# Kernel tuning notes

Measured on AMD Instinct MI355X. Metric: run time of the kernel, lower is better.

Reference implementation:

```python
import jax, jax.numpy as jnp
import numpy as np

D = 256      # input channels
DK = 64      # key/query/value channels
BS, W, H = 8, 64, 64


def setup_inputs() -> dict:
    key = jax.random.key(0)
    k1, k2, k3, k4 = jax.random.split(key, 4)
    v = jax.random.normal(k1, (BS, D, W, H), dtype=jnp.float32)
    # conv1x1 weights collapse to plain matrices over the channel dim
    Wqkv = jax.random.normal(k2, (3 * DK, D), dtype=jnp.float32) * 0.02
    Wout = jax.random.normal(k3, (D, DK), dtype=jnp.float32) * 0.02
    gamma = jax.random.normal(k4, (1,), dtype=jnp.float32)  # original inits to 0; nonzero for a non-degenerate baseline
    return {"v": v, "Wqkv": Wqkv, "Wout": Wout, "gamma": gamma}


def reference(v, Wqkv, Wout, gamma):
    bs, c, w, h = v.shape
    n = w * h
    d_k = Wout.shape[1]
    x = v.reshape(bs, c, n)                      # (b, c, n)
    qkv = jnp.einsum('oc,bcn->bon', Wqkv, x)      # 1x1 conv == channel matmul
    q = qkv[:, :d_k]                              # (b, dk, n)
    k = qkv[:, d_k:2 * d_k]
    val = qkv[:, 2 * d_k:]
    s = jnp.einsum('bdi,bdj->bij', q, k)          # (b, n, n) = query^T key
    beta = jax.nn.softmax(s, axis=2)              # exp(s - logsumexp(s, axis=2))
    y = jnp.einsum('bdi,bij->bdj', val, beta)     # bmm(value, beta)
    o = jnp.einsum('od,bdn->bon', Wout, y) * gamma[0] + x
    return o.reshape(bs, c, w, h)
```

## Files before the change

kernel.cpp:

```cpp
#include <hip/hip_runtime.h>

typedef unsigned short ushort_t;
typedef __bf16 bf16x8 __attribute__((ext_vector_type(8)));
typedef short short4v __attribute__((ext_vector_type(4)));
typedef float f32x4 __attribute__((ext_vector_type(4)));
typedef unsigned int uint4v __attribute__((ext_vector_type(4)));
typedef unsigned int uint2v __attribute__((ext_vector_type(2)));

#define NTOK 4096
#define DMODEL 256
#define DK 64
#define BS 8

__device__ __forceinline__ ushort_t f2bf(float f) {
  unsigned u = __builtin_bit_cast(unsigned, f);
  u += 0x7fffu + ((u >> 16) & 1u);
  return (ushort_t)(u >> 16);
}
__device__ __forceinline__ float bf2f(ushort_t s) {
  return __builtin_bit_cast(float, ((unsigned)s) << 16);
}
__device__ __forceinline__ bf16x8 lds_frag(const ushort_t* p) {
  return __builtin_bit_cast(bf16x8, *(const uint4v*)p);
}
__device__ __forceinline__ f32x4 mfma16(short4v a, short4v b, f32x4 c) {
#if defined(__HIP_DEVICE_COMPILE__)
#if __has_builtin(__builtin_amdgcn_mfma_f32_16x16x16bf16_1k)
  return __builtin_amdgcn_mfma_f32_16x16x16bf16_1k(a, b, c, 0, 0, 0);
#else
  typedef __bf16 bf16x4 __attribute__((ext_vector_type(4)));
  return __builtin_amdgcn_mfma_f32_16x16x16_bf16(__builtin_bit_cast(bf16x4, a),
                                                 __builtin_bit_cast(bf16x4, b), c, 0, 0, 0);
#endif
#else
  (void)a; (void)b;
  return c;
#endif
}

__global__ __launch_bounds__(256) void k_convert(const float* __restrict__ Wqkv,
                                                 const float* __restrict__ Wout,
                                                 ushort_t* __restrict__ Wb,
                                                 ushort_t* __restrict__ Woutb) {
  int i = blockIdx.x * 256 + threadIdx.x;
  if (i < 3 * DK * DMODEL) {
    Wb[i] = f2bf(Wqkv[i]);
  } else {
    int j = i - 3 * DK * DMODEL;
    Woutb[j] = f2bf(Wout[j]);
  }
}

__global__ __launch_bounds__(256) void k_transpose(const float* __restrict__ x,
                                                   ushort_t* __restrict__ xT) {
  const int b = blockIdx.z;
  const int c0 = blockIdx.y * 64;
  const int n0 = blockIdx.x * 64;
  const int tid = threadIdx.x;
  __shared__ __align__(16) ushort_t t[64 * 72];
  const float* xb = x + (size_t)b * DMODEL * NTOK;
  ushort_t* xTb = xT + (size_t)b * NTOK * DMODEL;
#pragma unroll
  for (int kr = 0; kr < 2; kr++) {
    int s = tid + 256 * kr;
    int c = s >> 3, ns = (s & 7) * 8;
    const float* src = xb + (size_t)(c0 + c) * NTOK + n0 + ns;
    f32x4 a = *(const f32x4*)src;
    f32x4 bq = *(const f32x4*)(src + 4);
    uint4v o;
    o.x = (unsigned)f2bf(a[0]) | ((unsigned)f2bf(a[1]) << 16);
    o.y = (unsigned)f2bf(a[2]) | ((unsigned)f2bf(a[3]) << 16);
    o.z = (unsigned)f2bf(bq[0]) | ((unsigned)f2bf(bq[1]) << 16);
    o.w = (unsigned)f2bf(bq[2]) | ((unsigned)f2bf(bq[3]) << 16);
    *(uint4v*)(t + c * 72 + ns) = o;
  }
  __syncthreads();
#pragma unroll
  for (int kr = 0; kr < 2; kr++) {
    int s = tid + 256 * kr;
    int n = s >> 3, cs = (s & 7) * 8;
    unsigned e0 = t[(cs + 0) * 72 + n], e1 = t[(cs + 1) * 72 + n];
    unsigned e2 = t[(cs + 2) * 72 + n], e3 = t[(cs + 3) * 72 + n];
    unsigned e4 = t[(cs + 4) * 72 + n], e5 = t[(cs + 5) * 72 + n];
    unsigned e6 = t[(cs + 6) * 72 + n], e7 = t[(cs + 7) * 72 + n];
    uint4v o;
    o.x = e0 | (e1 << 16); o.y = e2 | (e3 << 16);
    o.z = e4 | (e5 << 16); o.w = e6 | (e7 << 16);
    *(uint4v*)(xTb + (size_t)(n0 + n) * DMODEL + c0 + cs) = o;
  }
}

__global__ __launch_bounds__(256) void k_qkv(const ushort_t* __restrict__ xT,
                                             const ushort_t* __restrict__ W,
                                             ushort_t* __restrict__ QT,
                                             ushort_t* __restrict__ KT,
                                             ushort_t* __restrict__ Vv) {
  const int b = blockIdx.y;
  const int n0 = blockIdx.x * 64;
  const int tid = threadIdx.x;
  const int lane = tid & 63, wv = tid >> 6;
  const int quad = lane >> 4, l15 = lane & 15;
  __shared__ __align__(16) ushort_t lw[192 * 40];
  __shared__ __align__(16) ushort_t lx[64 * 40];
  f32x4 acc[3][4];
  const f32x4 zero4 = {0.f, 0.f, 0.f, 0.f};
#pragma unroll
  for (int i = 0; i < 3; i++)
#pragma unroll
    for (int j = 0; j < 4; j++) acc[i][j] = zero4;

  const ushort_t* xTb = xT + ((size_t)b * NTOK + n0) * DMODEL;

  for (int c0 = 0; c0 < DMODEL; c0 += 32) {
    __syncthreads();
#pragma unroll
    for (int kr = 0; kr < 3; kr++) {
      int s = tid + 256 * kr;
      int o = s >> 2, cs = (s & 3) * 8;
      *(uint4v*)(lw + o * 40 + cs) = *(const uint4v*)(W + o * DMODEL + c0 + cs);
    }
    {
      int n = tid >> 2, cs = (tid & 3) * 8;
      *(uint4v*)(lx + n * 40 + cs) = *(const uint4v*)(xTb + (size_t)n * DMODEL + c0 + cs);
    }
    __syncthreads();
    bf16x8 bb[4];
#pragma unroll
    for (int nt = 0; nt < 4; nt++) bb[nt] = lds_frag(lx + (nt * 16 + l15) * 40 + quad * 8);
#pragma unroll
    for (int mt = 0; mt < 3; mt++) {
      bf16x8 a = lds_frag(lw + (wv * 48 + mt * 16 + l15) * 40 + quad * 8);
#pragma unroll
      for (int nt = 0; nt < 4; nt++)
        acc[mt][nt] = __builtin_amdgcn_mfma_f32_16x16x32_bf16(a, bb[nt], acc[mt][nt], 0, 0, 0);
    }
  }
#pragma unroll
  for (int mt = 0; mt < 3; mt++) {
    int o = wv * 48 + mt * 16 + quad * 4;
#pragma unroll
    for (int nt = 0; nt < 4; nt++) {
      int n = n0 + nt * 16 + l15;
      f32x4 v4 = acc[mt][nt];
      if (o < 128) {
        ushort_t* dst = (o < 64) ? (QT + ((size_t)b * NTOK + n) * DK + o)
                                 : (KT + ((size_t)b * NTOK + n) * DK + (o - 64));
        uint2v ww;
        ww.x = (unsigned)f2bf(v4[0]) | ((unsigned)f2bf(v4[1]) << 16);
        ww.y = (unsigned)f2bf(v4[2]) | ((unsigned)f2bf(v4[3]) << 16);
        *(uint2v*)dst = ww;
      } else {
        int d = o - 128;
#pragma unroll
        for (int r = 0; r < 4; r++)
          Vv[((size_t)b * DK + d + r) * NTOK + n] = f2bf(v4[r]);
      }
    }
  }
}

__global__ __launch_bounds__(256) void k_stats(const ushort_t* __restrict__ QT,
                                               const ushort_t* __restrict__ KT,
                                               ushort_t* __restrict__ Vv) {
  const int b = blockIdx.y;
  const int i0 = blockIdx.x * 64;
  const int tid = threadIdx.x;
  const int lane = tid & 63, wv = tid >> 6;
  const int quad = lane >> 4, l15 = lane & 15;
  __shared__ __align__(16) ushort_t lq[64 * 72];
  __shared__ __align__(16) ushort_t lk[2][64 * 72];
  __shared__ float lrr[64];
  const ushort_t* QTb = QT + ((size_t)b * NTOK + i0) * DK;
  const ushort_t* KTb = KT + (size_t)b * NTOK * DK;
#pragma unroll
  for (int kr = 0; kr < 2; kr++) {
    int s = tid + 256 * kr;
    int row = s >> 3, ds = (s & 7) * 8;
    *(uint4v*)(lq + row * 72 + ds) = *(const uint4v*)(QTb + (size_t)row * DK + ds);
    *(uint4v*)(lk[0] + row * 72 + ds) = *(const uint4v*)(KTb + (size_t)row * DK + ds);
  }
  __syncthreads();
  bf16x8 a0 = lds_frag(lq + (wv * 16 + l15) * 72 + quad * 8);
  bf16x8 a1 = lds_frag(lq + (wv * 16 + l15) * 72 + 32 + quad * 8);
  float lsum0 = 0.f, lsum1 = 0.f, lsum2 = 0.f, lsum3 = 0.f;
  const f32x4 zero4 = {0.f, 0.f, 0.f, 0.f};
  for (int it = 0; it < 64; it++) {
    if (it + 1 < 64) {
      const ushort_t* src = KTb + (size_t)(it + 1) * 64 * DK;
      ushort_t* dstb = lk[(it + 1) & 1];
#pragma unroll
      for (int kr = 0; kr < 2; kr++) {
        int s = tid + 256 * kr;
        int row = s >> 3, ds = (s & 7) * 8;
        *(uint4v*)(dstb + row * 72 + ds) = *(const uint4v*)(src + (size_t)row * DK + ds);
      }
    }
    const ushort_t* kb = lk[it & 1];
#pragma unroll
    for (int nt = 0; nt < 4; nt++) {
      bf16x8 b0 = lds_frag(kb + (nt * 16 + l15) * 72 + quad * 8);
      bf16x8 b1 = lds_frag(kb + (nt * 16 + l15) * 72 + 32 + quad * 8);
      f32x4 s4 = __builtin_amdgcn_mfma_f32_16x16x32_bf16(a0, b0, zero4, 0, 0, 0);
      s4 = __builtin_amdgcn_mfma_f32_16x16x32_bf16(a1, b1, s4, 0, 0, 0);
      lsum0 += __expf(s4[0]);
      lsum1 += __expf(s4[1]);
      lsum2 += __expf(s4[2]);
      lsum3 += __expf(s4[3]);
    }
    __syncthreads();
  }
#pragma unroll
  for (int off = 1; off < 16; off <<= 1) {
    lsum0 += __shfl_xor(lsum0, off);
    lsum1 += __shfl_xor(lsum1, off);
    lsum2 += __shfl_xor(lsum2, off);
    lsum3 += __shfl_xor(lsum3, off);
  }
  if (l15 == 0) {
    int rr = wv * 16 + quad * 4;
    lrr[rr + 0] = 1.0f / lsum0;
    lrr[rr + 1] = 1.0f / lsum1;
    lrr[rr + 2] = 1.0f / lsum2;
    lrr[rr + 3] = 1.0f / lsum3;
  }
  __syncthreads();
  {
    int d = tid >> 2, ig = (tid & 3) * 16;
    ushort_t* vp = Vv + ((size_t)b * DK + d) * NTOK + i0 + ig;
    uint4v v0 = *(const uint4v*)vp;
    uint4v v1 = *(const uint4v*)(vp + 8);
    uint4v o0, o1;
    unsigned* vi0 = (unsigned*)&v0;
    unsigned* vi1 = (unsigned*)&v1;
    unsigned* oo0 = (unsigned*)&o0;
    unsigned* oo1 = (unsigned*)&o1;
#pragma unroll
    for (int w = 0; w < 4; w++) {
      float e0 = bf2f((ushort_t)(vi0[w] & 0xffff)) * lrr[ig + 2 * w];
      float e1 = bf2f((ushort_t)(vi0[w] >> 16)) * lrr[ig + 2 * w + 1];
      oo0[w] = (unsigned)f2bf(e0) | ((unsigned)f2bf(e1) << 16);
      float e2 = bf2f((ushort_t)(vi1[w] & 0xffff)) * lrr[ig + 8 + 2 * w];
      float e3 = bf2f((ushort_t)(vi1[w] >> 16)) * lrr[ig + 8 + 2 * w + 1];
      oo1[w] = (unsigned)f2bf(e2) | ((unsigned)f2bf(e3) << 16);
    }
    *(uint4v*)vp = o0;
    *(uint4v*)(vp + 8) = o1;
  }
}

__global__ __launch_bounds__(256) void k_attn(const ushort_t* __restrict__ QT,
                                              const ushort_t* __restrict__ KT,
                                              const ushort_t* __restrict__ Vv,
                                              const ushort_t* __restrict__ Wout,
                                              const float* __restrict__ gammap,
                                              const float* __restrict__ x,
                                              float* __restrict__ outp) {
  const int b = blockIdx.y;
  const int j0 = blockIdx.x * 64;
  const int tid = threadIdx.x;
  const int lane = tid & 63, wv = tid >> 6;
  const int quad = lane >> 4, l15 = lane & 15;

  __shared__ __align__(16) ushort_t pool[18432];
#define LQ(buf) (pool + (buf) * 4608)
#define LV(buf) (pool + 9216 + (buf) * 4608)
  float* rbuf = (float*)pool;
  ushort_t* pbuf = pool + 8704;

  const ushort_t* KTb = KT + ((size_t)b * NTOK + j0) * DK;
  const ushort_t* QTb = QT + (size_t)b * NTOK * DK;
  const ushort_t* Vb = Vv + (size_t)b * DK * NTOK;

#pragma unroll
  for (int kr = 0; kr < 2; kr++) {
    int s = tid + 256 * kr;
    int row = s >> 3, ds = (s & 7) * 8;
    *(uint4v*)(LQ(0) + row * 72 + ds) = *(const uint4v*)(KTb + (size_t)row * DK + ds);
  }
  __syncthreads();
  bf16x8 kb0[4], kb1[4];
#pragma unroll
  for (int nt = 0; nt < 4; nt++) {
    kb0[nt] = lds_frag(LQ(0) + (nt * 16 + l15) * 72 + quad * 8);
    kb1[nt] = lds_frag(LQ(0) + (nt * 16 + l15) * 72 + 32 + quad * 8);
  }
  __syncthreads();
#pragma unroll
  for (int kr = 0; kr < 2; kr++) {
    int s = tid + 256 * kr;
    int row = s >> 3, ds = (s & 7) * 8;
    *(uint4v*)(LQ(0) + row * 72 + ds) = *(const uint4v*)(QTb + (size_t)row * DK + ds);
    *(uint4v*)(LV(0) + row * 72 + ds) = *(const uint4v*)(Vb + (size_t)row * NTOK + ds);
  }
  __syncthreads();

  const f32x4 zero4 = {0.f, 0.f, 0.f, 0.f};
  f32x4 yt[4][4];
#pragma unroll
  for (int i = 0; i < 4; i++)
#pragma unroll
    for (int j = 0; j < 4; j++) yt[i][j] = zero4;

  for (int it = 0; it < 64; it++) {
    const int cb = it & 1, nb = cb ^ 1;
    const ushort_t* lqc = LQ(cb);
    const ushort_t* lvc = LV(cb);
    if (it + 1 < 64) {
      const ushort_t* qsrc = QTb + (size_t)(it + 1) * 64 * DK;
      const ushort_t* vsrc = Vb + (it + 1) * 64;
      ushort_t* lqn = LQ(nb);
      ushort_t* lvn = LV(nb);
#pragma unroll
      for (int kr = 0; kr < 2; kr++) {
        int s = tid + 256 * kr;
        int row = s >> 3, ds = (s & 7) * 8;
        *(uint4v*)(lqn + row * 72 + ds) = *(const uint4v*)(qsrc + (size_t)row * DK + ds);
        *(uint4v*)(lvn + row * 72 + ds) = *(const uint4v*)(vsrc + (size_t)row * NTOK + ds);
      }
    }
    bf16x8 a0 = lds_frag(lqc + (wv * 16 + l15) * 72 + quad * 8);
    bf16x8 a1 = lds_frag(lqc + (wv * 16 + l15) * 72 + 32 + quad * 8);
    short4v vf[4];
#pragma unroll
    for (int dsub = 0; dsub < 4; dsub++)
      vf[dsub] = __builtin_bit_cast(short4v,
          *(const uint2v*)(lvc + (dsub * 16 + l15) * 72 + wv * 16 + quad * 4));
#pragma unroll
    for (int nt = 0; nt < 4; nt++) {
      f32x4 s4 = __builtin_amdgcn_mfma_f32_16x16x32_bf16(a0, kb0[nt], zero4, 0, 0, 0);
      s4 = __builtin_amdgcn_mfma_f32_16x16x32_bf16(a1, kb1[nt], s4, 0, 0, 0);
      uint2v wp;
      wp.x = (unsigned)f2bf(__expf(s4[0])) | ((unsigned)f2bf(__expf(s4[1])) << 16);
      wp.y = (unsigned)f2bf(__expf(s4[2])) | ((unsigned)f2bf(__expf(s4[3])) << 16);
      short4v wf = __builtin_bit_cast(short4v, wp);
#pragma unroll
      for (int dsub = 0; dsub < 4; dsub++)
        yt[nt][dsub] = mfma16(wf, vf[dsub], yt[nt][dsub]);
    }
    __syncthreads();
  }

  if (wv == 0) {
#pragma unroll
    for (int nt = 0; nt < 4; nt++)
#pragma unroll
      for (int dsub = 0; dsub < 4; dsub++)
        *(f32x4*)(rbuf + (dsub * 16 + l15) * 68 + nt * 16 + quad * 4) = yt[nt][dsub];
  }
  __syncthreads();
  if (wv == 1) {
#pragma unroll
    for (int nt = 0; nt < 4; nt++)
#pragma unroll
      for (int dsub = 0; dsub < 4; dsub++) {
        float* p = rbuf + (dsub * 16 + l15) * 68 + nt * 16 + quad * 4;
        *(f32x4*)p = *(const f32x4*)p + yt[nt][dsub];
      }
  }
  __syncthreads();
  if (wv == 2) {
#pragma unroll
    for (int nt = 0; nt < 4; nt++)
#pragma unroll
      for (int dsub = 0; dsub < 4; dsub++) {
        float* p = rbuf + (dsub * 16 + l15) * 68 + nt * 16 + quad * 4;
        *(f32x4*)p = *(const f32x4*)p + yt[nt][dsub];
      }
  }
  __syncthreads();
  if (wv == 3) {
#pragma unroll
    for (int nt = 0; nt < 4; nt++)
#pragma unroll
      for (int dsub = 0; dsub < 4; dsub++) {
        const float* p = rbuf + (dsub * 16 + l15) * 68 + nt * 16 + quad * 4;
        f32x4 v4 = *(const f32x4*)p + yt[nt][dsub];
#pragma unroll
        for (int r = 0; r < 4; r++)
          pbuf[(nt * 16 + quad * 4 + r) * 72 + dsub * 16 + l15] = f2bf(v4[r]);
      }
  }
  __syncthreads();

  bf16x8 yb0[4], yb1[4];
#pragma unroll
  for (int nt = 0; nt < 4; nt++) {
    yb0[nt] = lds_frag(pbuf + (nt * 16 + l15) * 72 + quad * 8);
    yb1[nt] = lds_frag(pbuf + (nt * 16 + l15) * 72 + 32 + quad * 8);
  }
  f32x4 oacc[4][4];
#pragma unroll
  for (int m = 0; m < 4; m++)
#pragma unroll
    for (int nt = 0; nt < 4; nt++) oacc[m][nt] = zero4;
#pragma unroll
  for (int m = 0; m < 4; m++) {
    int c = (wv * 4 + m) * 16 + l15;
    bf16x8 aw0 = __builtin_bit_cast(bf16x8, *(const uint4v*)(Wout + c * DK + quad * 8));
    bf16x8 aw1 = __builtin_bit_cast(bf16x8, *(const uint4v*)(Wout + c * DK + 32 + quad * 8));
#pragma unroll
    for (int nt = 0; nt < 4; nt++) {
      oacc[m][nt] = __builtin_amdgcn_mfma_f32_16x16x32_bf16(aw0, yb0[nt], oacc[m][nt], 0, 0, 0);
      oacc[m][nt] = __builtin_amdgcn_mfma_f32_16x16x32_bf16(aw1, yb1[nt], oacc[m][nt], 0, 0, 0);
    }
  }
  float g = gammap[0];
  const float* xb = x + (size_t)b * DMODEL * NTOK;
  float* ob = outp + (size_t)b * DMODEL * NTOK;
#pragma unroll
  for (int m = 0; m < 4; m++) {
    int cbase = (wv * 4 + m) * 16 + quad * 4;
#pragma unroll
    for (int nt = 0; nt < 4; nt++) {
      int n = j0 + nt * 16 + l15;
#pragma unroll
      for (int r = 0; r < 4; r++) {
        size_t idx = (size_t)(cbase + r) * NTOK + n;
        ob[idx] = oacc[m][nt][r] * g + xb[idx];
      }
    }
  }
#undef LQ
#undef LV
}

extern "C" void kernel_launch(void* const* d_in, const int* in_sizes, int n_in,
                              void* d_out, int out_size, void* d_ws, size_t ws_size,
                              hipStream_t stream) {
  const float* v = (const float*)d_in[0];
  const float* Wqkv = (const float*)d_in[1];
  const float* Wout = (const float*)d_in[2];
  const float* gamma = (const float*)d_in[3];
  float* outp = (float*)d_out;

  ushort_t* xT = (ushort_t*)d_ws;
  ushort_t* QT = xT + (size_t)BS * NTOK * DMODEL;
  ushort_t* KT = QT + (size_t)BS * NTOK * DK;
  ushort_t* Vs = KT + (size_t)BS * NTOK * DK;
  ushort_t* Wb = Vs + (size_t)BS * DK * NTOK;
  ushort_t* Woutb = Wb + 3 * DK * DMODEL;

  k_convert<<<dim3(256), 256, 0, stream>>>(Wqkv, Wout, Wb, Woutb);
  k_transpose<<<dim3(64, 4, BS), 256, 0, stream>>>(v, xT);
  k_qkv<<<dim3(64, BS), 256, 0, stream>>>(xT, Wb, QT, KT, Vs);
  k_stats<<<dim3(64, BS), 256, 0, stream>>>(QT, KT, Vs);
  k_attn<<<dim3(64, BS), 256, 0, stream>>>(QT, KT, Vs, Woutb, gamma, v, outp);
}
```

Baseline: 221.9 us.

## Split attention key range across blocks, fold log2e into Q, use exp2

Both the row-sum pass and the PV pass now split the 4096-token reduction into two halves, launching 1024 blocks instead of 512 so more CUs are busy. Partial sums are merged in a small kernel and partial Y results are merged in a new output-projection kernel. Q weights are prescaled by 1/ln2 so the kernels can use the native exp2 instruction, and the normalization is applied to P in the PV loop instead of rescaling V in place. This adds two extra launches plus a bf16 partial-Y round trip through global memory, and it adds the bf16 rounding of the partial sums.

```diff
diff --git a/kernel.cpp b/kernel.cpp
--- a/kernel.cpp
+++ b/kernel.cpp
@@ -11,6 +11,7 @@
 #define DMODEL 256
 #define DK 64
 #define BS 8
+#define LN2INV 1.44269504088896f
 
 __device__ __forceinline__ ushort_t f2bf(float f) {
   unsigned u = __builtin_bit_cast(unsigned, f);
@@ -22,6 +23,17 @@
 }
 __device__ __forceinline__ bf16x8 lds_frag(const ushort_t* p) {
   return __builtin_bit_cast(bf16x8, *(const uint4v*)p);
+}
+__device__ __forceinline__ float fexp2(float x) {
+#if __has_builtin(__builtin_amdgcn_exp2f)
+  return __builtin_amdgcn_exp2f(x);
+#else
+  return exp2f(x);
+#endif
+}
+__device__ __forceinline__ unsigned bfpack(float x, float y) {
+  return __builtin_amdgcn_perm(__builtin_bit_cast(unsigned, y),
+                               __builtin_bit_cast(unsigned, x), 0x07060302u);
 }
 __device__ __forceinline__ f32x4 mfma16(short4v a, short4v b, f32x4 c) {
 #if defined(__HIP_DEVICE_COMPILE__)
@@ -44,7 +56,9 @@
                                                  ushort_t* __restrict__ Woutb) {
   int i = blockIdx.x * 256 + threadIdx.x;
   if (i < 3 * DK * DMODEL) {
-    Wb[i] = f2bf(Wqkv[i]);
+    float w = Wqkv[i];
+    if (i < DK * DMODEL) w *= LN2INV;
+    Wb[i] = f2bf(w);
   } else {
     int j = i - 3 * DK * DMODEL;
     Woutb[j] = f2bf(Wout[j]);
@@ -159,19 +173,21 @@
   }
 }
 
-__global__ __launch_bounds__(256) void k_stats(const ushort_t* __restrict__ QT,
-                                               const ushort_t* __restrict__ KT,
-                                               ushort_t* __restrict__ Vv) {
-  const int b = blockIdx.y;
-  const int i0 = blockIdx.x * 64;
+__global__ __launch_bounds__(256) void k_rsum(const ushort_t* __restrict__ QT,
+                                              const ushort_t* __restrict__ KT,
+                                              float* __restrict__ Rp) {
+  const int id = blockIdx.x;
+  const int b = id & 7;
+  const int rest = id >> 3;
+  const int i0 = (rest & 63) * 64;
+  const int jh = rest >> 6;
   const int tid = threadIdx.x;
   const int lane = tid & 63, wv = tid >> 6;
   const int quad = lane >> 4, l15 = lane & 15;
   __shared__ __align__(16) ushort_t lq[64 * 72];
   __shared__ __align__(16) ushort_t lk[2][64 * 72];
-  __shared__ float lrr[64];
   const ushort_t* QTb = QT + ((size_t)b * NTOK + i0) * DK;
-  const ushort_t* KTb = KT + (size_t)b * NTOK * DK;
+  const ushort_t* KTb = KT + ((size_t)b * NTOK + jh * 2048) * DK;
 #pragma unroll
   for (int kr = 0; kr < 2; kr++) {
     int s = tid + 256 * kr;
@@ -184,8 +200,8 @@
   bf16x8 a1 = lds_frag(lq + (wv * 16 + l15) * 72 + 32 + quad * 8);
   float lsum0 = 0.f, lsum1 = 0.f, lsum2 = 0.f, lsum3 = 0.f;
   const f32x4 zero4 = {0.f, 0.f, 0.f, 0.f};
-  for (int it = 0; it < 64; it++) {
-    if (it + 1 < 64) {
+  for (int it = 0; it < 32; it++) {
+    if (it + 1 < 32) {
       const ushort_t* src = KTb + (size_t)(it + 1) * 64 * DK;
       ushort_t* dstb = lk[(it + 1) & 1];
 #pragma unroll
@@ -202,10 +218,10 @@
       bf16x8 b1 = lds_frag(kb + (nt * 16 + l15) * 72 + 32 + quad * 8);
       f32x4 s4 = __builtin_amdgcn_mfma_f32_16x16x32_bf16(a0, b0, zero4, 0, 0, 0);
       s4 = __builtin_amdgcn_mfma_f32_16x16x32_bf16(a1, b1, s4, 0, 0, 0);
-      lsum0 += __expf(s4[0]);
-      lsum1 += __expf(s4[1]);
-      lsum2 += __expf(s4[2]);
-      lsum3 += __expf(s4[3]);
+      lsum0 += fexp2(s4[0]);
+      lsum1 += fexp2(s4[1]);
+      lsum2 += fexp2(s4[2]);
+      lsum3 += fexp2(s4[3]);
     }
     __syncthreads();
   }
@@ -216,47 +232,28 @@
     lsum2 += __shfl_xor(lsum2, off);
     lsum3 += __shfl_xor(lsum3, off);
   }
-  if (l15 == 0) {
-    int rr = wv * 16 + quad * 4;
-    lrr[rr + 0] = 1.0f / lsum0;
-    lrr[rr + 1] = 1.0f / lsum1;
-    lrr[rr + 2] = 1.0f / lsum2;
-    lrr[rr + 3] = 1.0f / lsum3;
-  }
-  __syncthreads();
-  {
-    int d = tid >> 2, ig = (tid & 3) * 16;
-    ushort_t* vp = Vv + ((size_t)b * DK + d) * NTOK + i0 + ig;
-    uint4v v0 = *(const uint4v*)vp;
-    uint4v v1 = *(const uint4v*)(vp + 8);
-    uint4v o0, o1;
-    unsigned* vi0 = (unsigned*)&v0;
-    unsigned* vi1 = (unsigned*)&v1;
-    unsigned* oo0 = (unsigned*)&o0;
-    unsigned* oo1 = (unsigned*)&o1;
-#pragma unroll
-    for (int w = 0; w < 4; w++) {
-      float e0 = bf2f((ushort_t)(vi0[w] & 0xffff)) * lrr[ig + 2 * w];
-      float e1 = bf2f((ushort_t)(vi0[w] >> 16)) * lrr[ig + 2 * w + 1];
-      oo0[w] = (unsigned)f2bf(e0) | ((unsigned)f2bf(e1) << 16);
-      float e2 = bf2f((ushort_t)(vi1[w] & 0xffff)) * lrr[ig + 8 + 2 * w];
-      float e3 = bf2f((ushort_t)(vi1[w] >> 16)) * lrr[ig + 8 + 2 * w + 1];
-      oo1[w] = (unsigned)f2bf(e2) | ((unsigned)f2bf(e3) << 16);
-    }
-    *(uint4v*)vp = o0;
-    *(uint4v*)(vp + 8) = o1;
-  }
-}
-
-__global__ __launch_bounds__(256) void k_attn(const ushort_t* __restrict__ QT,
-                                              const ushort_t* __restrict__ KT,
-                                              const ushort_t* __restrict__ Vv,
-                                              const ushort_t* __restrict__ Wout,
-                                              const float* __restrict__ gammap,
-                                              const float* __restrict__ x,
-                                              float* __restrict__ outp) {
-  const int b = blockIdx.y;
-  const int j0 = blockIdx.x * 64;
+  if (l15 < 4) {
+    float v = (l15 == 0) ? lsum0 : (l15 == 1) ? lsum1 : (l15 == 2) ? lsum2 : lsum3;
+    Rp[((size_t)(jh * 8 + b)) * NTOK + i0 + wv * 16 + quad * 4 + l15] = v;
+  }
+}
+
+__global__ __launch_bounds__(256) void k_rmerge(const float* __restrict__ Rp,
+                                                float* __restrict__ Rr) {
+  int g = blockIdx.x * 256 + threadIdx.x;
+  Rr[g] = 1.0f / (Rp[g] + Rp[BS * NTOK + g]);
+}
+
+__global__ __launch_bounds__(256) void k_pv(const ushort_t* __restrict__ QT,
+                                            const ushort_t* __restrict__ KT,
+                                            const ushort_t* __restrict__ Vv,
+                                            const float* __restrict__ Rr,
+                                            ushort_t* __restrict__ Yp) {
+  const int id = blockIdx.x;
+  const int b = id & 7;
+  const int rest = id >> 3;
+  const int j0 = (rest & 63) * 64;
+  const int ih = rest >> 6;
   const int tid = threadIdx.x;
   const int lane = tid & 63, wv = tid >> 6;
   const int quad = lane >> 4, l15 = lane & 15;
@@ -268,8 +265,9 @@
   ushort_t* pbuf = pool + 8704;
 
   const ushort_t* KTb = KT + ((size_t)b * NTOK + j0) * DK;
-  const ushort_t* QTb = QT + (size_t)b * NTOK * DK;
-  const ushort_t* Vb = Vv + (size_t)b * DK * NTOK;
+  const ushort_t* QTb = QT + ((size_t)b * NTOK + ih * 2048) * DK;
+  const ushort_t* Vbb = Vv + (size_t)b * DK * NTOK + ih * 2048;
+  const float* Rrb = Rr + (size_t)b * NTOK + ih * 2048;
 
 #pragma unroll
   for (int kr = 0; kr < 2; kr++) {
@@ -290,7 +288,7 @@
     int s = tid + 256 * kr;
     int row = s >> 3, ds = (s & 7) * 8;
     *(uint4v*)(LQ(0) + row * 72 + ds) = *(const uint4v*)(QTb + (size_t)row * DK + ds);
-    *(uint4v*)(LV(0) + row * 72 + ds) = *(const uint4v*)(Vb + (size_t)row * NTOK + ds);
+    *(uint4v*)(LV(0) + row * 72 + ds) = *(const uint4v*)(Vbb + (size_t)row * NTOK + ds);
   }
   __syncthreads();
 
@@ -301,37 +299,34 @@
 #pragma unroll
     for (int j = 0; j < 4; j++) yt[i][j] = zero4;
 
-  for (int it = 0; it < 64; it++) {
+  for (int it = 0; it < 32; it++) {
     const int cb = it & 1, nb = cb ^ 1;
-    const ushort_t* lqc = LQ(cb);
-    const ushort_t* lvc = LV(cb);
-    if (it + 1 < 64) {
+    f32x4 rv = *(const f32x4*)(Rrb + it * 64 + wv * 16 + quad * 4);
+    if (it + 1 < 32) {
       const ushort_t* qsrc = QTb + (size_t)(it + 1) * 64 * DK;
-      const ushort_t* vsrc = Vb + (it + 1) * 64;
-      ushort_t* lqn = LQ(nb);
-      ushort_t* lvn = LV(nb);
 #pragma unroll
       for (int kr = 0; kr < 2; kr++) {
         int s = tid + 256 * kr;
         int row = s >> 3, ds = (s & 7) * 8;
-        *(uint4v*)(lqn + row * 72 + ds) = *(const uint4v*)(qsrc + (size_t)row * DK + ds);
-        *(uint4v*)(lvn + row * 72 + ds) = *(const uint4v*)(vsrc + (size_t)row * NTOK + ds);
-      }
-    }
-    bf16x8 a0 = lds_frag(lqc + (wv * 16 + l15) * 72 + quad * 8);
-    bf16x8 a1 = lds_frag(lqc + (wv * 16 + l15) * 72 + 32 + quad * 8);
+        *(uint4v*)(LQ(nb) + row * 72 + ds) = *(const uint4v*)(qsrc + (size_t)row * DK + ds);
+        *(uint4v*)(LV(nb) + row * 72 + ds) =
+            *(const uint4v*)(Vbb + (size_t)row * NTOK + (it + 1) * 64 + ds);
+      }
+    }
+    bf16x8 a0 = lds_frag(LQ(cb) + (wv * 16 + l15) * 72 + quad * 8);
+    bf16x8 a1 = lds_frag(LQ(cb) + (wv * 16 + l15) * 72 + 32 + quad * 8);
     short4v vf[4];
 #pragma unroll
     for (int dsub = 0; dsub < 4; dsub++)
       vf[dsub] = __builtin_bit_cast(short4v,
-          *(const uint2v*)(lvc + (dsub * 16 + l15) * 72 + wv * 16 + quad * 4));
+          *(const uint2v*)(LV(cb) + (dsub * 16 + l15) * 72 + wv * 16 + quad * 4));
 #pragma unroll
     for (int nt = 0; nt < 4; nt++) {
       f32x4 s4 = __builtin_amdgcn_mfma_f32_16x16x32_bf16(a0, kb0[nt], zero4, 0, 0, 0);
       s4 = __builtin_amdgcn_mfma_f32_16x16x32_bf16(a1, kb1[nt], s4, 0, 0, 0);
       uint2v wp;
-      wp.x = (unsigned)f2bf(__expf(s4[0])) | ((unsigned)f2bf(__expf(s4[1])) << 16);
-      wp.y = (unsigned)f2bf(__expf(s4[2])) | ((unsigned)f2bf(__expf(s4[3])) << 16);
+      wp.x = bfpack(fexp2(s4[0]) * rv[0], fexp2(s4[1]) * rv[1]);
+      wp.y = bfpack(fexp2(s4[2]) * rv[2], fexp2(s4[3]) * rv[3]);
       short4v wf = __builtin_bit_cast(short4v, wp);
 #pragma unroll
       for (int dsub = 0; dsub < 4; dsub++)
@@ -382,6 +377,53 @@
   }
   __syncthreads();
 
+  ushort_t* Ypb = Yp + ((size_t)(ih * 8 + b) * NTOK + j0) * DK;
+#pragma unroll
+  for (int kr = 0; kr < 2; kr++) {
+    int s = tid + 256 * kr;
+    int row = s >> 3, c8 = (s & 7) * 8;
+    *(uint4v*)(Ypb + (size_t)row * DK + c8) = *(const uint4v*)(pbuf + row * 72 + c8);
+  }
+#undef LQ
+#undef LV
+}
+
+__global__ __launch_bounds__(256) void k_out(const ushort_t* __restrict__ Yp,
+                                             const ushort_t* __restrict__ Wout,
+                                             const float* __restrict__ gammap,
+                                             const float* __restrict__ x,
+                                             float* __restrict__ outp) {
+  const int id = blockIdx.x;
+  const int b = id & 7;
+  const int n0 = (id >> 3) * 64;
+  const int tid = threadIdx.x;
+  const int lane = tid & 63, wv = tid >> 6;
+  const int quad = lane >> 4, l15 = lane & 15;
+  __shared__ __align__(16) ushort_t pbuf[64 * 72];
+
+  const ushort_t* Y0 = Yp + ((size_t)b * NTOK + n0) * DK;
+  const ushort_t* Y1 = Yp + ((size_t)(8 + b) * NTOK + n0) * DK;
+#pragma unroll
+  for (int kr = 0; kr < 2; kr++) {
+    int s = tid + 256 * kr;
+    int row = s >> 3, c8 = (s & 7) * 8;
+    uint4v ua = *(const uint4v*)(Y0 + (size_t)row * DK + c8);
+    uint4v ub = *(const uint4v*)(Y1 + (size_t)row * DK + c8);
+    uint4v oc;
+    unsigned* pa = (unsigned*)&ua;
+    unsigned* pb = (unsigned*)&ub;
+    unsigned* po = (unsigned*)&oc;
+#pragma unroll
+    for (int w = 0; w < 4; w++) {
+      float lo = bf2f((ushort_t)(pa[w] & 0xffff)) + bf2f((ushort_t)(pb[w] & 0xffff));
+      float hi = bf2f((ushort_t)(pa[w] >> 16)) + bf2f((ushort_t)(pb[w] >> 16));
+      po[w] = bfpack(lo, hi);
+    }
+    *(uint4v*)(pbuf + row * 72 + c8) = oc;
+  }
+  __syncthreads();
+
+  const f32x4 zero4 = {0.f, 0.f, 0.f, 0.f};
   bf16x8 yb0[4], yb1[4];
 #pragma unroll
   for (int nt = 0; nt < 4; nt++) {
@@ -412,7 +454,7 @@
     int cbase = (wv * 4 + m) * 16 + quad * 4;
 #pragma unroll
     for (int nt = 0; nt < 4; nt++) {
-      int n = j0 + nt * 16 + l15;
+      int n = n0 + nt * 16 + l15;
 #pragma unroll
       for (int r = 0; r < 4; r++) {
         size_t idx = (size_t)(cbase + r) * NTOK + n;
@@ -420,8 +462,6 @@
       }
     }
   }
-#undef LQ
-#undef LV
 }
 
 extern "C" void kernel_launch(void* const* d_in, const int* in_sizes, int n_in,
@@ -439,10 +479,15 @@
   ushort_t* Vs = KT + (size_t)BS * NTOK * DK;
   ushort_t* Wb = Vs + (size_t)BS * DK * NTOK;
   ushort_t* Woutb = Wb + 3 * DK * DMODEL;
+  float* Rp = (float*)(Woutb + DMODEL * DK);
+  float* Rr = Rp + 2 * (size_t)BS * NTOK;
+  ushort_t* Yp = (ushort_t*)(Rr + (size_t)BS * NTOK);
 
   k_convert<<<dim3(256), 256, 0, stream>>>(Wqkv, Wout, Wb, Woutb);
   k_transpose<<<dim3(64, 4, BS), 256, 0, stream>>>(v, xT);
   k_qkv<<<dim3(64, BS), 256, 0, stream>>>(xT, Wb, QT, KT, Vs);
-  k_stats<<<dim3(64, BS), 256, 0, stream>>>(QT, KT, Vs);
-  k_attn<<<dim3(64, BS), 256, 0, stream>>>(QT, KT, Vs, Woutb, gamma, v, outp);
-}
+  k_rsum<<<dim3(1024), 256, 0, stream>>>(QT, KT, Rp);
+  k_rmerge<<<dim3(128), 256, 0, stream>>>(Rp, Rr);
+  k_pv<<<dim3(1024), 256, 0, stream>>>(QT, KT, Vs, Rr, Yp);
+  k_out<<<dim3(512), 256, 0, stream>>>(Yp, Woutb, gamma, v, outp);
+}
```

Result: faster. 215.8 us (-2.8%).
